# Performance work log

Hardware: AMD Instinct MI355X
Metric: run time of the kernel (lower is better)

## Reference

```python
import jax, jax.numpy as jnp
import numpy as np

NUM_CLASSES = 6
GROUP = 256
TEMP = 2.0
LAM = 0.8  # soft_lambda mixing rotation vs translation label distance


def _rnc_core(feat, label_dist, t):
    # Rank-N-Contrast: for anchor i, positive j (j!=i), denominator over k with
    # label_dist[i,k] >= label_dist[i,j], k != i.  feat [n,d], label_dist [n,n].
    n = feat.shape[0]
    diff = feat[:, None, :] - feat[None, :, :]
    dist = jnp.sqrt(jnp.sum(diff * diff, axis=-1) + 1e-12)  # [n,n] l2 feature distance
    logits = -dist / t
    logits = logits - jax.lax.stop_gradient(jnp.max(logits, axis=1, keepdims=True))
    exp_logits = jnp.exp(logits)
    eye = jnp.eye(n, dtype=bool)
    # mask[i,j,k]: k belongs to the denominator set of anchor i / positive j
    mask = (label_dist[:, None, :] >= label_dist[:, :, None]) & (~eye)[:, None, :]
    denom = jnp.einsum('ijk,ik->ij', mask.astype(feat.dtype), exp_logits)  # [n,n]
    log_prob = logits - jnp.log(denom)
    return -jnp.sum(jnp.where(eye, 0.0, log_prob)) / (n * (n - 1))


def _l1_pair(x):
    # pairwise l1 distance summed over last dim: [n,n]
    return jnp.sum(jnp.abs(x[:, None, :] - x[None, :, :]), axis=-1)


def _loss_sym(feat, green, trans):
    L = LAM * _l1_pair(green) + (1.0 - LAM) * _l1_pair(trans)
    return _rnc_core(feat, L, TEMP)


def _loss_nonsym(feat, green, red, trans):
    rot = 0.5 * (_l1_pair(green) + _l1_pair(red))
    L = LAM * rot + (1.0 - LAM) * _l1_pair(trans)
    return _rnc_core(feat, L, TEMP)


def _loss_mug(feat, green, red, trans, sym):
    nonsym = (sym[:, 0] == 0).astype(feat.dtype)
    both = nonsym[:, None] * nonsym[None, :]  # red axis only matters when both non-sym
    rot = (_l1_pair(green) + both * _l1_pair(red)) / (1.0 + both)
    L = LAM * rot + (1.0 - LAM) * _l1_pair(trans)
    return _rnc_core(feat, L, TEMP)


def setup_inputs() -> dict:
    key = jax.random.key(0)
    ks = jax.random.split(key, 4)
    B = NUM_CLASSES * GROUP
    D = 256
    features = jax.random.normal(ks[0], (B, D), dtype=jnp.float32)
    labels = jnp.repeat(jnp.arange(NUM_CLASSES, dtype=jnp.int32), GROUP)

    def unit(k, shape):
        v = jax.random.normal(k, shape, dtype=jnp.float32)
        return v / jnp.linalg.norm(v, axis=-1, keepdims=True)

    gt_green = unit(ks[1], (B, 3))
    gt_red = unit(ks[2], (B, 3))
    gt_trans = jax.random.normal(ks[3], (B, 3), dtype=jnp.float32)
    # sym flags: classes 0,1 fully symmetric (sym[:,0]==1 everywhere -> rnc_loss);
    # classes 2,3,4 have sym[:,0]==0 -> nonSym branch; class 5 (mug) mixed flags.
    sym0 = np.ones((B,), dtype=np.int32)
    for c in (2, 3, 4):
        sym0[c * GROUP:(c + 1) * GROUP] = 0
    sym0[5 * GROUP:5 * GROUP + GROUP // 2] = 0
    sym = np.zeros((B, 4), dtype=np.int32)
    sym[:, 0] = sym0
    return {"features": features, "labels": labels, "gt_green": gt_green,
            "gt_red": gt_red, "gt_trans": gt_trans, "sym": jnp.asarray(sym)}


def reference(features, labels, gt_green, gt_red, gt_trans, sym):
    # labels are sorted into NUM_CLASSES equal contiguous groups of size GROUP,
    # so the per-unique-label gather becomes static slicing.
    total = jnp.float32(0.0)
    for c in range(NUM_CLASSES):
        s = slice(c * GROUP, (c + 1) * GROUP)
        f, g, r, t, sy = features[s], gt_green[s], gt_red[s], gt_trans[s], sym[s]
        if c == 5:
            total = total + _loss_mug(f, g, r, t, sy)
        elif c in (0, 1):  # no sym[:,0]==0 entries -> symmetric RnC loss
            total = total + _loss_sym(f, g, t)
        else:
            total = total + _loss_nonsym(f, g, r, t)
    return total / NUM_CLASSES
```

## Files before the change

kernel.cpp:

```cpp
#include <hip/hip_runtime.h>
#include <cmath>

#define NCLS 6
#define GRP 256
#define DIM 256
#define NBLK (NCLS * 64)


__global__ __launch_bounds__(256) void transpose_kernel(
    const float* __restrict__ feat, float* __restrict__ ft,
    unsigned int* __restrict__ counter)
{
    __shared__ float tile[64][65];
    const int b  = blockIdx.x;
    const int c  = b >> 4;
    const int tt = b & 15;
    const int r0 = (tt >> 2) << 6;
    const int c0 = (tt & 3) << 6;
    const int t  = threadIdx.x;

    if (b == 0 && t == 0)
        __hip_atomic_store(counter, 0u, __ATOMIC_RELAXED, __HIP_MEMORY_SCOPE_AGENT);

    #pragma unroll
    for (int q = 0; q < 4; ++q) {
        int idx  = q * 256 + t;
        int row  = idx >> 4;
        int col4 = (idx & 15) << 2;
        float4 v = *reinterpret_cast<const float4*>(
            feat + (size_t)(c * 256 + r0 + row) * DIM + c0 + col4);
        tile[row][col4 + 0] = v.x; tile[row][col4 + 1] = v.y;
        tile[row][col4 + 2] = v.z; tile[row][col4 + 3] = v.w;
    }
    __syncthreads();
    #pragma unroll
    for (int q = 0; q < 4; ++q) {
        int idx = q * 256 + t;
        int dd  = idx >> 4;
        int r4  = (idx & 15) << 2;
        float4 o = make_float4(tile[r4][dd], tile[r4 + 1][dd],
                               tile[r4 + 2][dd], tile[r4 + 3][dd]);
        *reinterpret_cast<float4*>(
            ft + (size_t)(c * 256 + c0 + dd) * GRP + r0 + r4) = o;
    }
}

__global__ __launch_bounds__(512) void rnc_main_kernel(
    const float* __restrict__ ft,
    const float* __restrict__ feat,
    const float* __restrict__ green,
    const float* __restrict__ red,
    const float* __restrict__ trans,
    const int*   __restrict__ sym,
    float* __restrict__ partial,
    unsigned int* __restrict__ counter,
    float* __restrict__ out)
{
    __shared__ __align__(16) float4 fi4[2][128];
    __shared__ float part[2][4][GRP];
    __shared__ __align__(16) float2 LEs[4][GRP];
    __shared__ float lgs[4][GRP];
    __shared__ __align__(16) float pdn[4][GRP][2];
    __shared__ float rbuf[8];
    __shared__ int iswin;

    const int b    = blockIdx.x;
    const int c    = b >> 6;
    const int a0   = (b & 63) << 2;
    const int base = c << 8;
    const int a0g  = base + a0;
    const int t    = threadIdx.x;

    if (t < 256) {
        float x0 = feat[(size_t)(a0g + 0) * DIM + t];
        float x1 = feat[(size_t)(a0g + 1) * DIM + t];
        float x2 = feat[(size_t)(a0g + 2) * DIM + t];
        float x3 = feat[(size_t)(a0g + 3) * DIM + t];
        fi4[t >> 7][t & 127] = make_float4(x0, x1, x2, x3);
    }
    __syncthreads();

    const int col = t & 255;
    const int dh  = t >> 8;

    {
        const float*  cp = ft + (size_t)((c << 8) + (dh << 7)) * GRP + col;
        const float4* fb = fi4[dh];
        float ac0 = 0.f, ac1 = 0.f, ac2 = 0.f, ac3 = 0.f;
        #pragma unroll 8
        for (int d = 0; d < 128; ++d) {
            float v  = cp[(size_t)d * GRP];
            float4 f = fb[d];
            float x;
            x = f.x - v; ac0 = fmaf(x, x, ac0);
            x = f.y - v; ac1 = fmaf(x, x, ac1);
            x = f.z - v; ac2 = fmaf(x, x, ac2);
            x = f.w - v; ac3 = fmaf(x, x, ac3);
        }
        part[dh][0][col] = ac0;
        part[dh][1][col] = ac1;
        part[dh][2][col] = ac2;
        part[dh][3][col] = ac3;
    }
    __syncthreads();

    {
        const int kg = base + col;
        float kgx = green[3*kg], kgy = green[3*kg+1], kgz = green[3*kg+2];
        float ktx = trans[3*kg], kty = trans[3*kg+1], ktz = trans[3*kg+2];
        float krx = 0.f, kry = 0.f, krz = 0.f;
        int ksym = 0;
        if (c >= 2) { krx = red[3*kg]; kry = red[3*kg+1]; krz = red[3*kg+2]; }
        if (c == 5) ksym = sym[4*kg];

        #pragma unroll
        for (int e = 0; e < 2; ++e) {
            const int p  = dh + 2 * e;
            const int ag = a0g + p;
            float s  = part[0][p][col] + part[1][p][col];
            float lg = -0.5f * sqrtf(s + 1e-12f);

            float l1g = fabsf(green[3*ag] - kgx) + fabsf(green[3*ag+1] - kgy)
                      + fabsf(green[3*ag+2] - kgz);
            float l1t = fabsf(trans[3*ag] - ktx) + fabsf(trans[3*ag+1] - kty)
                      + fabsf(trans[3*ag+2] - ktz);
            float L;
            if (c < 2) {
                L = 0.8f * l1g + 0.2f * l1t;
            } else {
                float l1r = fabsf(red[3*ag] - krx) + fabsf(red[3*ag+1] - kry)
                          + fabsf(red[3*ag+2] - krz);
                float rot;
                if (c < 5) {
                    rot = 0.5f * (l1g + l1r);
                } else {
                    float both = ((sym[4*ag] == 0) && (ksym == 0)) ? 1.f : 0.f;
                    rot = (l1g + both * l1r) / (1.f + both);
                }
                L = 0.8f * rot + 0.2f * l1t;
            }
            LEs[p][col] = make_float2(L, __expf(lg));
            lgs[p][col] = lg;
        }
    }
    __syncthreads();

    const int w  = t >> 6;
    const int l  = t & 63;
    const int p  = w & 3;
    const int hh = w >> 2;

    float L0 = LEs[p][l].x;
    float L1 = LEs[p][l + 64].x;
    float L2 = LEs[p][l + 128].x;
    float L3 = LEs[p][l + 192].x;

    const float4* q4 = reinterpret_cast<const float4*>(LEs[p]);
    float dn0 = 0.f, dn1 = 0.f, dn2 = 0.f, dn3 = 0.f;
    #pragma unroll 8
    for (int q = hh * 64; q < hh * 64 + 64; ++q) {
        float4 u = q4[q];
        dn0 += (u.x >= L0) ? u.y : 0.f;  dn0 += (u.z >= L0) ? u.w : 0.f;
        dn1 += (u.x >= L1) ? u.y : 0.f;  dn1 += (u.z >= L1) ? u.w : 0.f;
        dn2 += (u.x >= L2) ? u.y : 0.f;  dn2 += (u.z >= L2) ? u.w : 0.f;
        dn3 += (u.x >= L3) ? u.y : 0.f;  dn3 += (u.z >= L3) ? u.w : 0.f;
    }
    pdn[p][l][hh]       = dn0;
    pdn[p][l + 64][hh]  = dn1;
    pdn[p][l + 128][hh] = dn2;
    pdn[p][l + 192][hh] = dn3;
    __syncthreads();

    float acc = 0.f;
    #pragma unroll
    for (int e = 0; e < 2; ++e) {
        int idx = t + e * 512;
        int pp  = idx >> 8;
        int j   = idx & 255;
        float dn = pdn[pp][j][0] + pdn[pp][j][1];
        float v  = lgs[pp][j] - __logf(dn);
        acc += (j != a0 + pp) ? v : 0.f;
    }
    #pragma unroll
    for (int off = 32; off > 0; off >>= 1)
        acc += __shfl_xor(acc, off);
    if (l == 0) rbuf[w] = acc;
    __syncthreads();
    if (t == 0) {
        float s = 0.f;
        #pragma unroll
        for (int k = 0; k < 8; ++k) s += rbuf[k];
        __hip_atomic_store(&partial[b], s, __ATOMIC_RELAXED, __HIP_MEMORY_SCOPE_AGENT);
        unsigned int old = __hip_atomic_fetch_add(counter, 1u, __ATOMIC_ACQ_REL,
                                                  __HIP_MEMORY_SCOPE_AGENT);
        iswin = (old == NBLK - 1) ? 1 : 0;
    }
    __syncthreads();

    if (iswin) {
        float a2 = 0.f;
        if (t < NBLK)
            a2 = __hip_atomic_load(&partial[t], __ATOMIC_RELAXED, __HIP_MEMORY_SCOPE_AGENT);
        #pragma unroll
        for (int off = 32; off > 0; off >>= 1)
            a2 += __shfl_xor(a2, off);
        if (l == 0) rbuf[w] = a2;
        __syncthreads();
        if (t == 0) {
            float s = 0.f;
            #pragma unroll
            for (int k = 0; k < 8; ++k) s += rbuf[k];
            out[0] = -s / (256.f * 255.f * 6.f);
        }
    }
}

extern "C" void kernel_launch(void* const* d_in, const int* in_sizes, int n_in,
                              void* d_out, int out_size, void* d_ws, size_t ws_size,
                              hipStream_t stream)
{
    const float* feat  = (const float*)d_in[0];
    const float* green = (const float*)d_in[2];
    const float* red   = (const float*)d_in[3];
    const float* trans = (const float*)d_in[4];
    const int*   sym   = (const int*)d_in[5];

    float*        wsf     = (float*)d_ws;
    float*        partial = wsf;
    unsigned int* counter = (unsigned int*)(wsf + 512);
    float*        ft      = wsf + 2048;
    float*        out     = (float*)d_out;

    transpose_kernel<<<NCLS * 16, 256, 0, stream>>>(feat, ft, counter);
    rnc_main_kernel<<<NBLK, 512, 0, stream>>>(ft, feat, green, red, trans, sym,
                                              partial, counter, out);
}
```

Measured before the change: 31.21 us.

## Fuse transpose into main kernel with grid-wide spin barrier

Folds the separate transpose kernel into the main kernel. Each of the 384 blocks transposes one 32x32 tile of the features, then all blocks wait on a global atomic counter before computing distances. Anchor features are now read straight from global memory instead of being staged in shared memory. The final reduction moves to block 0, which spins on a second counter, and both counters are zeroed with a hipMemsetAsync. This removes a kernel launch boundary, but only works if all 384 blocks are resident at once (risk of deadlock) and adds a memset launch plus spin-wait cost.

```diff
diff --git a/kernel.cpp b/kernel.cpp
--- a/kernel.cpp
+++ b/kernel.cpp
@@ -4,65 +4,26 @@
 #define NCLS 6
 #define GRP 256
 #define DIM 256
-#define NBLK (NCLS * 64)
-
-
-__global__ __launch_bounds__(256) void transpose_kernel(
-    const float* __restrict__ feat, float* __restrict__ ft,
-    unsigned int* __restrict__ counter)
-{
-    __shared__ float tile[64][65];
-    const int b  = blockIdx.x;
-    const int c  = b >> 4;
-    const int tt = b & 15;
-    const int r0 = (tt >> 2) << 6;
-    const int c0 = (tt & 3) << 6;
-    const int t  = threadIdx.x;
-
-    if (b == 0 && t == 0)
-        __hip_atomic_store(counter, 0u, __ATOMIC_RELAXED, __HIP_MEMORY_SCOPE_AGENT);
-
-    #pragma unroll
-    for (int q = 0; q < 4; ++q) {
-        int idx  = q * 256 + t;
-        int row  = idx >> 4;
-        int col4 = (idx & 15) << 2;
-        float4 v = *reinterpret_cast<const float4*>(
-            feat + (size_t)(c * 256 + r0 + row) * DIM + c0 + col4);
-        tile[row][col4 + 0] = v.x; tile[row][col4 + 1] = v.y;
-        tile[row][col4 + 2] = v.z; tile[row][col4 + 3] = v.w;
-    }
-    __syncthreads();
-    #pragma unroll
-    for (int q = 0; q < 4; ++q) {
-        int idx = q * 256 + t;
-        int dd  = idx >> 4;
-        int r4  = (idx & 15) << 2;
-        float4 o = make_float4(tile[r4][dd], tile[r4 + 1][dd],
-                               tile[r4 + 2][dd], tile[r4 + 3][dd]);
-        *reinterpret_cast<float4*>(
-            ft + (size_t)(c * 256 + c0 + dd) * GRP + r0 + r4) = o;
-    }
-}
-
-__global__ __launch_bounds__(512) void rnc_main_kernel(
-    const float* __restrict__ ft,
+#define NBLK 384
+
+
+__global__ __launch_bounds__(512, 4) void rnc_fused_kernel(
     const float* __restrict__ feat,
     const float* __restrict__ green,
     const float* __restrict__ red,
     const float* __restrict__ trans,
     const int*   __restrict__ sym,
+    float* __restrict__ ft,
     float* __restrict__ partial,
-    unsigned int* __restrict__ counter,
+    unsigned int* __restrict__ ctr,
     float* __restrict__ out)
 {
-    __shared__ __align__(16) float4 fi4[2][128];
+    __shared__ float ttile[32][33];
     __shared__ float part[2][4][GRP];
     __shared__ __align__(16) float2 LEs[4][GRP];
     __shared__ float lgs[4][GRP];
     __shared__ __align__(16) float pdn[4][GRP][2];
     __shared__ float rbuf[8];
-    __shared__ int iswin;
 
     const int b    = blockIdx.x;
     const int c    = b >> 6;
@@ -71,12 +32,33 @@
     const int a0g  = base + a0;
     const int t    = threadIdx.x;
 
-    if (t < 256) {
-        float x0 = feat[(size_t)(a0g + 0) * DIM + t];
-        float x1 = feat[(size_t)(a0g + 1) * DIM + t];
-        float x2 = feat[(size_t)(a0g + 2) * DIM + t];
-        float x3 = feat[(size_t)(a0g + 3) * DIM + t];
-        fi4[t >> 7][t & 127] = make_float4(x0, x1, x2, x3);
+    {
+        const int tr = ((b & 63) >> 3) << 5;
+        const int tc = (b & 7) << 5;
+        #pragma unroll
+        for (int e = 0; e < 2; ++e) {
+            int idx = (e << 9) + t;
+            int r   = idx >> 5;
+            int cc  = idx & 31;
+            ttile[r][cc] = feat[(size_t)(base + tr + r) * DIM + tc + cc];
+        }
+        __syncthreads();
+        #pragma unroll
+        for (int e = 0; e < 2; ++e) {
+            int idx = (e << 9) + t;
+            int dd  = idx >> 5;
+            int kk  = idx & 31;
+            ft[(size_t)(base + tc + dd) * GRP + tr + kk] = ttile[kk][dd];
+        }
+    }
+
+    __syncthreads();
+    if (t == 0) {
+        __threadfence();
+        __hip_atomic_fetch_add(&ctr[0], 1u, __ATOMIC_ACQ_REL, __HIP_MEMORY_SCOPE_AGENT);
+        while (__hip_atomic_load(&ctr[0], __ATOMIC_ACQUIRE, __HIP_MEMORY_SCOPE_AGENT)
+               < (unsigned)NBLK)
+            __builtin_amdgcn_s_sleep(2);
     }
     __syncthreads();
 
@@ -84,18 +66,17 @@
     const int dh  = t >> 8;
 
     {
-        const float*  cp = ft + (size_t)((c << 8) + (dh << 7)) * GRP + col;
-        const float4* fb = fi4[dh];
+        const float* cp = ft + (size_t)(base + (dh << 7)) * GRP + col;
+        const float* f0 = feat + (size_t)a0g * DIM + (dh << 7);
         float ac0 = 0.f, ac1 = 0.f, ac2 = 0.f, ac3 = 0.f;
         #pragma unroll 8
         for (int d = 0; d < 128; ++d) {
-            float v  = cp[(size_t)d * GRP];
-            float4 f = fb[d];
+            float v = cp[(size_t)d * GRP];
             float x;
-            x = f.x - v; ac0 = fmaf(x, x, ac0);
-            x = f.y - v; ac1 = fmaf(x, x, ac1);
-            x = f.z - v; ac2 = fmaf(x, x, ac2);
-            x = f.w - v; ac3 = fmaf(x, x, ac3);
+            x = f0[d]       - v; ac0 = fmaf(x, x, ac0);
+            x = f0[d + 256] - v; ac1 = fmaf(x, x, ac1);
+            x = f0[d + 512] - v; ac2 = fmaf(x, x, ac2);
+            x = f0[d + 768] - v; ac3 = fmaf(x, x, ac3);
         }
         part[dh][0][col] = ac0;
         part[dh][1][col] = ac1;
@@ -191,13 +172,16 @@
         #pragma unroll
         for (int k = 0; k < 8; ++k) s += rbuf[k];
         __hip_atomic_store(&partial[b], s, __ATOMIC_RELAXED, __HIP_MEMORY_SCOPE_AGENT);
-        unsigned int old = __hip_atomic_fetch_add(counter, 1u, __ATOMIC_ACQ_REL,
-                                                  __HIP_MEMORY_SCOPE_AGENT);
-        iswin = (old == NBLK - 1) ? 1 : 0;
-    }
-    __syncthreads();
-
-    if (iswin) {
+        __hip_atomic_fetch_add(&ctr[1], 1u, __ATOMIC_RELEASE, __HIP_MEMORY_SCOPE_AGENT);
+    }
+
+    if (b == 0) {
+        if (t == 0) {
+            while (__hip_atomic_load(&ctr[1], __ATOMIC_ACQUIRE, __HIP_MEMORY_SCOPE_AGENT)
+                   < (unsigned)NBLK)
+                __builtin_amdgcn_s_sleep(2);
+        }
+        __syncthreads();
         float a2 = 0.f;
         if (t < NBLK)
             a2 = __hip_atomic_load(&partial[t], __ATOMIC_RELAXED, __HIP_MEMORY_SCOPE_AGENT);
@@ -227,11 +211,11 @@
 
     float*        wsf     = (float*)d_ws;
     float*        partial = wsf;
-    unsigned int* counter = (unsigned int*)(wsf + 512);
+    unsigned int* ctr     = (unsigned int*)(wsf + 448);
     float*        ft      = wsf + 2048;
     float*        out     = (float*)d_out;
 
-    transpose_kernel<<<NCLS * 16, 256, 0, stream>>>(feat, ft, counter);
-    rnc_main_kernel<<<NBLK, 512, 0, stream>>>(ft, feat, green, red, trans, sym,
-                                              partial, counter, out);
+    hipMemsetAsync(ctr, 0, 2 * sizeof(unsigned int), stream);
+    rnc_fused_kernel<<<NBLK, 512, 0, stream>>>(feat, green, red, trans, sym,
+                                               ft, partial, ctr, out);
 }
```

Result: slower. 77.08 us (+146.9%).
